# Optimization experiments

Hardware: AMD Instinct MI355X
Metric: run time of the kernel (lower is better)

## Reference

```python
import jax, jax.numpy as jnp
import numpy as np

B, T, C, H = 8, 1024, 1024, 16  # batch, seq, n_embd, n_head


def setup_inputs() -> dict:
    key = jax.random.key(0)
    ks = jax.random.split(key, 5)
    scale = 1.0 / np.sqrt(C)
    return {
        "x": jax.random.normal(ks[0], (B, T, C), dtype=jnp.float32),
        "Wqkv": jax.random.normal(ks[1], (C, 3 * C), dtype=jnp.float32) * scale,
        "bqkv": jax.random.normal(ks[2], (3 * C,), dtype=jnp.float32) * 0.02,
        "Wproj": jax.random.normal(ks[3], (C, C), dtype=jnp.float32) * scale,
        "bproj": jax.random.normal(ks[4], (C,), dtype=jnp.float32) * 0.02,
        "n_head": H,
    }


def reference(x, Wqkv, bqkv, Wproj, bproj, n_head):
    Bb, Tt, Cc = x.shape
    hd = Cc // n_head  # head dim
    qkv = x @ Wqkv + bqkv                      # [B,T,3C]
    q, k, v = jnp.split(qkv, 3, axis=-1)       # each [B,T,C]
    # [B,T,C] -> [B,H,T,hd]
    def to_heads(t):
        return t.reshape(Bb, Tt, n_head, hd).transpose(0, 2, 1, 3)
    q, k, v = to_heads(q), to_heads(k), to_heads(v)
    scores = jnp.einsum("bhqd,bhkd->bhqk", q, k) / jnp.sqrt(jnp.asarray(hd, q.dtype))
    causal = jnp.tril(jnp.ones((Tt, Tt), dtype=bool))
    scores = jnp.where(causal, scores, jnp.asarray(-jnp.inf, scores.dtype))
    attn = jax.nn.softmax(scores, axis=-1)
    y = jnp.einsum("bhqk,bhkd->bhqd", attn, v)  # [B,H,T,hd]
    y = y.transpose(0, 2, 1, 3).reshape(Bb, Tt, Cc)
    return y @ Wproj + bproj
```

## Files before the change

### kernel.cpp

```cpp
#include <hip/hip_runtime.h>
#include <hip/hip_bf16.h>
#include <math.h>
#include <type_traits>

#define Bz 8
#define Tz 1024
#define Cz 1024
#define Hz 16
#define HDz 64
#define Mz (Bz*Tz)
#define N1 (3*Cz)
#define QKN 2048

typedef __attribute__((ext_vector_type(8))) short short8;
typedef __attribute__((ext_vector_type(4))) short short4v;
typedef __attribute__((ext_vector_type(4))) float floatx4;

template<int V> using IC = std::integral_constant<int, V>;

__device__ __forceinline__ unsigned short f2bf(float f) {
    unsigned u = __float_as_uint(f);
    return (unsigned short)((u + 0x7FFFu + ((u >> 16) & 1u)) >> 16);
}

__device__ __forceinline__ unsigned pkbf(float a, float b) {
    __hip_bfloat162 h = __float22bfloat162_rn(make_float2(a, b));
    return *(unsigned*)&h;
}

__device__ __forceinline__ void gload16(const void* g, void* l) {
    __builtin_amdgcn_global_load_lds(
        (const __attribute__((address_space(1))) unsigned int*)g,
        (__attribute__((address_space(3))) unsigned int*)l, 16, 0, 0);
}

__global__ __launch_bounds__(256) void prep_kernel(
    const float* __restrict__ x, unsigned short* __restrict__ xb,
    const float* __restrict__ Wqkv, unsigned short* __restrict__ Wqkvt,
    const float* __restrict__ Wproj, unsigned short* __restrict__ Wprojt)
{
    __shared__ float tile[32][33];
    const int bid = blockIdx.x;
    const int tid = threadIdx.x;
    if (bid < 8192) {
        int i = bid * 256 + tid;
        float4 v = *(const float4*)&x[(size_t)i * 4];
        ushort4 o;
        o.x = f2bf(v.x); o.y = f2bf(v.y); o.z = f2bf(v.z); o.w = f2bf(v.w);
        *(ushort4*)&xb[(size_t)i * 4] = o;
        return;
    }
    const float* W; unsigned short* Wt; int K, N, n0, k0;
    if (bid < 11264) {
        int b = bid - 8192;  W = Wqkv;  Wt = Wqkvt;  K = Cz; N = N1;
        n0 = (b % 96) * 32;  k0 = (b / 96) * 32;
    } else {
        int b = bid - 11264; W = Wproj; Wt = Wprojt; K = Cz; N = Cz;
        n0 = (b % 32) * 32;  k0 = (b / 32) * 32;
    }
    const int tx = tid & 31, ty = tid >> 5;
#pragma unroll
    for (int i = 0; i < 4; ++i)
        tile[ty + i * 8][tx] = W[(size_t)(k0 + ty + i * 8) * N + n0 + tx];
    __syncthreads();
#pragma unroll
    for (int i = 0; i < 4; ++i)
        Wt[(size_t)(n0 + ty + i * 8) * K + k0 + tx] = f2bf(tile[tx][ty + i * 8]);
}

__global__ __launch_bounds__(512, 4) void gemm128_qkv(
    const unsigned short* __restrict__ A,
    const unsigned short* __restrict__ Bt,
    const float* __restrict__ bias,
    unsigned short* __restrict__ Cqk, unsigned short* __restrict__ VtG)
{
    __shared__ unsigned short lds[2 * 20480];
    constexpr int NT = 16;

    const int tid = threadIdx.x;
    const int lane = tid & 63;
    const int w = tid >> 6;
    const int wm = w >> 2, wn = w & 3;
    const int quad = lane >> 4, m16 = lane & 15;
    const int sw7 = m16 & 7;

    int wg = blockIdx.x;
    wg = (wg & 7) * 128 + (wg >> 3);
    const int bx = wg & 15, by = wg >> 4;
    const int row0 = by * 128, col0 = bx * 192;

    const int srow = tid >> 3;
    const int scol = ((tid & 7) ^ (srow & 7)) * 8;
    const unsigned short* a0 = A  + (size_t)(row0 + srow) * Cz + scol;
    const unsigned short* b0 = Bt + (size_t)(col0 + srow) * Cz + scol;

    auto stageA = [&](int kt, int db) {
        unsigned short* d = &lds[db * 20480 + w * 512];
        gload16(a0 + kt * 64, d);
        gload16(a0 + kt * 64 + 64 * Cz, d + 4096);
    };
    auto stageB = [&](int kt, int db) {
        unsigned short* d = &lds[db * 20480 + 8192 + w * 512];
        gload16(b0 + kt * 64, d);
        gload16(b0 + kt * 64 + 64 * Cz, d + 4096);
        gload16(b0 + kt * 64 + 128 * Cz, d + 8192);
    };

    float bv[3];
#pragma unroll
    for (int ni = 0; ni < 3; ++ni)
        bv[ni] = bias[col0 + wn * 48 + ni * 16 + m16];
    asm volatile("s_waitcnt vmcnt(0)" ::: "memory");

    floatx4 acc[4][3];
#pragma unroll
    for (int mi = 0; mi < 4; ++mi)
#pragma unroll
        for (int ni = 0; ni < 3; ++ni)
            acc[mi][ni] = (floatx4){0.f, 0.f, 0.f, 0.f};

    stageA(0, 0); stageB(0, 0);
    stageB(1, 1);
    asm volatile("s_waitcnt vmcnt(3)" ::: "memory");
    asm volatile("s_barrier" ::: "memory");

    int b = 0;
#pragma unroll 1
    for (int kt = 0; kt < NT; ++kt, b ^= 1) {
        const unsigned short* lA = &lds[b * 20480];
        const unsigned short* lB = &lds[b * 20480 + 8192];

        short8 bfr[3][2];
#pragma unroll
        for (int ni = 0; ni < 3; ++ni) {
            const int rb = wn * 48 + ni * 16 + m16;
#pragma unroll
            for (int ks = 0; ks < 2; ++ks)
                bfr[ni][ks] = *(const short8*)&lB[(rb >> 6) * 4096 + (rb & 63) * 64
                                                  + ((((ks << 2) | quad) ^ sw7) << 3)];
        }
        short8 af[2][2];
#pragma unroll
        for (int jj = 0; jj < 2; ++jj)
#pragma unroll
            for (int ks = 0; ks < 2; ++ks)
                af[jj][ks] = *(const short8*)&lA[wm * 4096 + (jj * 16 + m16) * 64
                                                 + ((((ks << 2) | quad) ^ sw7) << 3)];
        if (kt + 1 < NT) stageA(kt + 1, b ^ 1);
        asm volatile("s_barrier" ::: "memory");
        asm volatile("s_waitcnt lgkmcnt(0)" ::: "memory");
        __builtin_amdgcn_sched_barrier(0);
        __builtin_amdgcn_s_setprio(1);
#pragma unroll
        for (int ks = 0; ks < 2; ++ks)
#pragma unroll
            for (int jj = 0; jj < 2; ++jj)
#pragma unroll
                for (int ni = 0; ni < 3; ++ni)
                    acc[jj][ni] = __builtin_amdgcn_mfma_f32_16x16x32_bf16(
                        af[jj][ks], bfr[ni][ks], acc[jj][ni], 0, 0, 0);
        __builtin_amdgcn_s_setprio(0);
        asm volatile("s_barrier" ::: "memory");

        short8 af2[2][2];
#pragma unroll
        for (int jj = 0; jj < 2; ++jj)
#pragma unroll
            for (int ks = 0; ks < 2; ++ks)
                af2[jj][ks] = *(const short8*)&lA[wm * 4096 + ((2 + jj) * 16 + m16) * 64
                                                  + ((((ks << 2) | quad) ^ sw7) << 3)];
        if (kt + 2 < NT) stageB(kt + 2, b);
        asm volatile("s_barrier" ::: "memory");
        asm volatile("s_waitcnt lgkmcnt(0)" ::: "memory");
        __builtin_amdgcn_sched_barrier(0);
        __builtin_amdgcn_s_setprio(1);
#pragma unroll
        for (int ks = 0; ks < 2; ++ks)
#pragma unroll
            for (int jj = 0; jj < 2; ++jj)
#pragma unroll
                for (int ni = 0; ni < 3; ++ni)
                    acc[2 + jj][ni] = __builtin_amdgcn_mfma_f32_16x16x32_bf16(
                        af2[jj][ks], bfr[ni][ks], acc[2 + jj][ni], 0, 0, 0);
        __builtin_amdgcn_s_setprio(0);
        if (kt < NT - 2) { asm volatile("s_waitcnt vmcnt(3)" ::: "memory"); }
        else             { asm volatile("s_waitcnt vmcnt(0)" ::: "memory"); }
        asm volatile("s_barrier" ::: "memory");
    }

#pragma unroll
    for (int ni = 0; ni < 3; ++ni) {
        const int c0 = col0 + wn * 48 + ni * 16;
        if (c0 < 2048) {
#pragma unroll
            for (int mi = 0; mi < 4; ++mi)
#pragma unroll
                for (int reg = 0; reg < 4; ++reg) {
                    const int r = row0 + wm * 64 + mi * 16 + quad * 4 + reg;
                    Cqk[(size_t)r * QKN + c0 + m16] = f2bf(acc[mi][ni][reg] + bv[ni]);
                }
        } else {
            const int cb = c0 - 2048;
            const int hsel = cb >> 6;
            const int dd = (cb & 63) + m16;
            const int bq = row0 >> 10;
            const int tb = row0 & 1023;
            unsigned short* drow = VtG
                + (size_t)(bq * Hz + hsel) * (HDz * Tz)
                + (size_t)dd * Tz + tb;
#pragma unroll
            for (int mi = 0; mi < 4; ++mi) {
                const int t = wm * 64 + mi * 16 + quad * 4;
                unsigned pk[2];
                pk[0] = pkbf(acc[mi][ni][0] + bv[ni], acc[mi][ni][1] + bv[ni]);
                pk[1] = pkbf(acc[mi][ni][2] + bv[ni], acc[mi][ni][3] + bv[ni]);
                *(uint2*)&drow[t] = *(uint2*)pk;
            }
        }
    }
}

template<int NI, int MODE, int NXB>
__global__ __launch_bounds__(512) void gemm8p(
    const unsigned short* __restrict__ A,
    const unsigned short* __restrict__ Bt,
    const float* __restrict__ bias,
    void* __restrict__ Cout, unsigned short* __restrict__ VtG)
{
    constexpr int LDSB = 16384 + NI * 4096;
    constexpr int NT = 16;
    constexpr int NBLK = (Mz / 256) * NXB;
    constexpr int CHUNK = NBLK / 8;
    constexpr int NOUT = NXB * NI * 64;
    __shared__ unsigned short lds[2 * LDSB];

    const int tid = threadIdx.x;
    const int lane = tid & 63;
    const int w = tid >> 6;
    const int wm = w >> 2, wn = w & 3;
    const int quad = lane >> 4, m16 = lane & 15;
    const int sw7 = m16 & 7;

    int wg = blockIdx.x;
    wg = (wg & 7) * CHUNK + (wg >> 3);
    const int bx = wg % NXB, by = wg / NXB;
    const int row0 = by * 256, col0 = bx * (NI * 64);

    const int srow = tid >> 3;
    const int scol = ((tid & 7) ^ (srow & 7)) * 8;
    const unsigned short* sA[2][2];
    const unsigned short* sBu[NI];
#pragma unroll
    for (int h = 0; h < 2; ++h)
#pragma unroll
        for (int c = 0; c < 2; ++c)
            sA[h][c] = A + (size_t)(row0 + h * 128 + c * 64 + srow) * Cz + scol;
#pragma unroll
    for (int u = 0; u < NI; ++u)
        sBu[u] = Bt + (size_t)(col0 + u * 64 + srow) * Cz + scol;

    auto stage_tile = [&](int kt, int db) {
        unsigned short* base = &lds[db * LDSB];
#pragma unroll
        for (int u = 0; u < NI; ++u)
            gload16(sBu[u] + kt * 64, base + 16384 + u * 4096 + w * 512);
        gload16(sA[0][0] + kt * 64, base + w * 512);
        gload16(sA[0][1] + kt * 64, base + w * 512 + 4096);
        gload16(sA[1][0] + kt * 64, base + 8192 + w * 512);
        gload16(sA[1][1] + kt * 64, base + 8192 + w * 512 + 4096);
    };

    float bv[NI];
#pragma unroll
    for (int ni = 0; ni < NI; ++ni)
        bv[ni] = bias[col0 + wn * (NI * 16) + ni * 16 + m16];
    asm volatile("s_waitcnt vmcnt(0)" ::: "memory");

    floatx4 acc[8][NI];
#pragma unroll
    for (int mi = 0; mi < 8; ++mi)
#pragma unroll
        for (int ni = 0; ni < NI; ++ni)
            acc[mi][ni] = (floatx4){0.f, 0.f, 0.f, 0.f};

    stage_tile(0, 0);
    stage_tile(1, 1);

    int b = 0;
#pragma unroll 1
    for (int kt = 0; kt < NT; ++kt, b ^= 1) {
        if (kt < NT - 1) {
            if constexpr (NI == 3) asm volatile("s_waitcnt vmcnt(7)" ::: "memory");
            else                   asm volatile("s_waitcnt vmcnt(6)" ::: "memory");
        } else {
            asm volatile("s_waitcnt vmcnt(0)" ::: "memory");
        }
        asm volatile("s_barrier" ::: "memory");

        const unsigned short* lA = &lds[b * LDSB];
        const unsigned short* lB = &lds[b * LDSB + 16384];

        auto loadA = [&](auto pc, short8 (&af)[2][2]) {
            constexpr int p = decltype(pc)::value;
            constexpr int hf = p >> 1;
#pragma unroll
            for (int j = 0; j < 2; ++j) {
                const int ra = ((p & 1) * 64 + j * 32 + wm * 16 + m16) * 64;
#pragma unroll
                for (int ks = 0; ks < 2; ++ks)
                    af[j][ks] = *(const short8*)&lA[hf * 8192 + ra + ((((ks << 2) | quad) ^ sw7) << 3)];
            }
        };

        short8 bfr[NI][2];
#pragma unroll
        for (int ni = 0; ni < NI; ++ni) {
            const int rb = (wn * (NI * 16) + ni * 16 + m16) * 64;
#pragma unroll
            for (int ks = 0; ks < 2; ++ks)
                bfr[ni][ks] = *(const short8*)&lB[rb + ((((ks << 2) | quad) ^ sw7) << 3)];
        }

        auto cluster = [&](auto pc, short8 (&af)[2][2]) {
            constexpr int p = decltype(pc)::value;
            __builtin_amdgcn_s_setprio(1);
#pragma unroll
            for (int ks = 0; ks < 2; ++ks)
#pragma unroll
                for (int j = 0; j < 2; ++j)
#pragma unroll
                    for (int ni = 0; ni < NI; ++ni)
                        acc[p * 2 + j][ni] = __builtin_amdgcn_mfma_f32_16x16x32_bf16(
                            af[j][ks], bfr[ni][ks], acc[p * 2 + j][ni], 0, 0, 0);
            __builtin_amdgcn_s_setprio(0);
        };

        short8 afA[2][2], afB[2][2];
        loadA(IC<0>{}, afA);
        __builtin_amdgcn_sched_barrier(0);
        loadA(IC<1>{}, afB);
        __builtin_amdgcn_sched_barrier(0);
        asm volatile("s_waitcnt lgkmcnt(4)" ::: "memory");
        __builtin_amdgcn_sched_barrier(0);
        cluster(IC<0>{}, afA);
        loadA(IC<2>{}, afA);
        __builtin_amdgcn_sched_barrier(0);
        asm volatile("s_waitcnt lgkmcnt(4)" ::: "memory");
        __builtin_amdgcn_sched_barrier(0);
        cluster(IC<1>{}, afB);
        loadA(IC<3>{}, afB);
        __builtin_amdgcn_sched_barrier(0);
        asm volatile("s_waitcnt lgkmcnt(4)" ::: "memory");
        __builtin_amdgcn_sched_barrier(0);
        cluster(IC<2>{}, afA);
        asm volatile("s_waitcnt lgkmcnt(0)" ::: "memory");
        __builtin_amdgcn_sched_barrier(0);
        if (kt + 2 < NT) {
            asm volatile("s_barrier" ::: "memory");
            stage_tile(kt + 2, b);
        }
        __builtin_amdgcn_sched_barrier(0);
        cluster(IC<3>{}, afB);
    }

    if constexpr (MODE == 0) {
#pragma unroll
        for (int ni = 0; ni < NI; ++ni) {
            const int c = col0 + wn * (NI * 16) + ni * 16 + m16;
#pragma unroll
            for (int mi = 0; mi < 8; ++mi)
#pragma unroll
                for (int reg = 0; reg < 4; ++reg) {
                    const int r = row0 + mi * 32 + wm * 16 + quad * 4 + reg;
                    ((float*)Cout)[(size_t)r * NOUT + c] = acc[mi][ni][reg] + bv[ni];
                }
        }
    } else {
#pragma unroll
        for (int ni = 0; ni < NI; ++ni) {
            const int c0 = col0 + wn * (NI * 16) + ni * 16;
            if (c0 < 2048) {
#pragma unroll
                for (int mi = 0; mi < 8; ++mi)
#pragma unroll
                    for (int reg = 0; reg < 4; ++reg) {
                        const int r = row0 + mi * 32 + wm * 16 + quad * 4 + reg;
                        ((unsigned short*)Cout)[(size_t)r * QKN + c0 + m16] =
                            f2bf(acc[mi][ni][reg] + bv[ni]);
                    }
            } else {
                const int cb = c0 - 2048;
                const int hsel = cb >> 6;
                const int dd = (cb & 63) + m16;
                const int bq = row0 >> 10;
                const int tb = row0 & 1023;
                unsigned short* drow = VtG
                    + (size_t)(bq * Hz + hsel) * (HDz * Tz)
                    + (size_t)dd * Tz + tb;
#pragma unroll
                for (int mi = 0; mi < 8; ++mi) {
                    const int t = mi * 32 + wm * 16 + quad * 4;
                    unsigned pk[2];
                    pk[0] = pkbf(acc[mi][ni][0] + bv[ni], acc[mi][ni][1] + bv[ni]);
                    pk[1] = pkbf(acc[mi][ni][2] + bv[ni], acc[mi][ni][3] + bv[ni]);
                    *(uint2*)&drow[t] = *(uint2*)pk;
                }
            }
        }
    }
}

__global__ __launch_bounds__(128) void attn_kernel(const unsigned short* __restrict__ qkb,
    const unsigned short* __restrict__ VtG, unsigned short* __restrict__ attb)
{
    __shared__ unsigned short Ks[2][64 * 64];
    __shared__ unsigned short Vs[2][64 * 64];

    const int bid = blockIdx.x;
    const int qi = 15 - (bid >> 7);
    const int bh = bid & 127;
    const int b = bh >> 4, h = bh & 15;
    const int tid = threadIdx.x, lane = tid & 63, w = tid >> 6;
    const int quad = lane >> 4, m16 = lane & 15;

    const unsigned short* Kb = qkb + (size_t)(b * Tz) * QKN + Cz + h * HDz;
    const unsigned short* Vb = VtG + (size_t)bh * (HDz * Tz);

    const int l3 = lane >> 3, l7 = lane & 7;
    const int gsw = ((l7 ^ l3) << 3);
    const int sw = m16 & 7;
    const int p0 = (quad ^ sw) << 3;

    short8 onesf = (short8){0,0,0,0,0,0,0,0};
    if (m16 == 0) {
        const short one = (short)0x3F80;
        onesf = (short8){one,one,one,one,one,one,one,one};
    }

    int srow[4];
#pragma unroll
    for (int i = 0; i < 4; ++i) srow[i] = w * 32 + i * 8 + l3;

#pragma unroll
    for (int i = 0; i < 4; ++i) {
        gload16(Kb + (size_t)srow[i] * QKN + gsw, &Ks[0][(w * 4 + i) * 512]);
        gload16(Vb + (size_t)srow[i] * Tz + gsw, &Vs[0][(w * 4 + i) * 512]);
    }

    short8 qf[2][2];
    int qrow[2];
#pragma unroll
    for (int mi = 0; mi < 2; ++mi) {
        qrow[mi] = qi * 64 + w * 32 + mi * 16 + m16;
        const size_t rq = (size_t)(b * Tz + qrow[mi]) * QKN + h * HDz;
        qf[mi][0] = *(const short8*)&qkb[rq + quad * 8];
        qf[mi][1] = *(const short8*)&qkb[rq + 32 + quad * 8];
    }

    floatx4 of[2][4];
#pragma unroll
    for (int mi = 0; mi < 2; ++mi)
#pragma unroll
        for (int dc = 0; dc < 4; ++dc) of[mi][dc] = (floatx4){0.f, 0.f, 0.f, 0.f};
    floatx4 lsum[2];
    lsum[0] = (floatx4){0.f, 0.f, 0.f, 0.f};
    lsum[1] = (floatx4){0.f, 0.f, 0.f, 0.f};

    int buf = 0;

    auto tile_body = [&](auto diag_c) {
        constexpr bool DIAG = decltype(diag_c)::value;
        short8 pf[2][2];
#pragma unroll
        for (int m0 = 0; m0 < 4; ++m0) {
            if (DIAG && w == 0 && m0 >= 2) continue;
            const unsigned short* kr = &Ks[buf][(m0 * 16 + m16) * 64];
            short8 kf0 = *(const short8*)&kr[p0];
            short8 kf1 = *(const short8*)&kr[p0 ^ 32];
#pragma unroll
            for (int mi = 0; mi < 2; ++mi) {
                floatx4 st = (floatx4){0.f, 0.f, 0.f, 0.f};
                st = __builtin_amdgcn_mfma_f32_16x16x32_bf16(kf0, qf[mi][0], st, 0, 0, 0);
                st = __builtin_amdgcn_mfma_f32_16x16x32_bf16(kf1, qf[mi][1], st, 0, 0, 0);
                float p[4];
#pragma unroll
                for (int reg = 0; reg < 4; ++reg) {
                    p[reg] = exp2f(st[reg] * 0.18033688f);
                    if (DIAG) {
                        int key = m0 * 16 + quad * 4 + reg;
                        int qr  = w * 32 + mi * 16 + m16;
                        p[reg] = (key <= qr) ? p[reg] : 0.f;
                    }
                }
                unsigned* pp = (unsigned*)&pf[mi][m0 >> 1];
                pp[(m0 & 1) * 2 + 0] = pkbf(p[0], p[1]);
                pp[(m0 & 1) * 2 + 1] = pkbf(p[2], p[3]);
            }
        }
#pragma unroll
        for (int kg = 0; kg < 2; ++kg) {
            if (DIAG && w == 0 && kg == 1) continue;
#pragma unroll
            for (int mi = 0; mi < 2; ++mi)
                lsum[mi] = __builtin_amdgcn_mfma_f32_16x16x32_bf16(onesf, pf[mi][kg], lsum[mi], 0, 0, 0);
#pragma unroll
            for (int dc = 0; dc < 4; ++dc) {
                const unsigned short* vrow = &Vs[buf][(dc * 16 + m16) * 64];
                const int g0 = kg * 4 + (quad >> 1);
                const int off = (quad & 1) * 4;
                short4v v0 = *(const short4v*)&vrow[((g0 ^ sw) << 3) + off];
                short4v v1 = *(const short4v*)&vrow[(((g0 + 2) ^ sw) << 3) + off];
                short8 vf;
                vf[0] = v0[0]; vf[1] = v0[1]; vf[2] = v0[2]; vf[3] = v0[3];
                vf[4] = v1[0]; vf[5] = v1[1]; vf[6] = v1[2]; vf[7] = v1[3];
#pragma unroll
                for (int mi = 0; mi < 2; ++mi)
                    of[mi][dc] = __builtin_amdgcn_mfma_f32_16x16x32_bf16(vf, pf[mi][kg], of[mi][dc], 0, 0, 0);
            }
        }
    };

    for (int ki = 0; ki <= qi; ++ki) {
        __syncthreads();
        if (ki < qi) {
            const size_t ko = (size_t)(ki + 1) * 64;
#pragma unroll
            for (int i = 0; i < 4; ++i) {
                gload16(Kb + (ko + srow[i]) * QKN + gsw, &Ks[buf ^ 1][(w * 4 + i) * 512]);
                gload16(Vb + (size_t)srow[i] * Tz + ko + gsw, &Vs[buf ^ 1][(w * 4 + i) * 512]);
            }
        }
        if (ki == qi) tile_body(std::true_type{});
        else          tile_body(std::false_type{});
        buf ^= 1;
    }

#pragma unroll
    for (int mi = 0; mi < 2; ++mi) {
        const float l = __shfl(lsum[mi][0], m16);
        const float inv = 1.f / l;
        const size_t orow = (size_t)(b * Tz + qrow[mi]) * Cz + h * HDz;
#pragma unroll
        for (int dc = 0; dc < 4; ++dc) {
            ushort4 o;
            o.x = f2bf(of[mi][dc][0] * inv);
            o.y = f2bf(of[mi][dc][1] * inv);
            o.z = f2bf(of[mi][dc][2] * inv);
            o.w = f2bf(of[mi][dc][3] * inv);
            *(ushort4*)&attb[orow + dc * 16 + quad * 4] = o;
        }
    }
}

extern "C" void kernel_launch(void* const* d_in, const int* in_sizes, int n_in,
                              void* d_out, int out_size, void* d_ws, size_t ws_size,
                              hipStream_t stream)
{
    const float* x     = (const float*)d_in[0];
    const float* Wqkv  = (const float*)d_in[1];
    const float* bqkv  = (const float*)d_in[2];
    const float* Wproj = (const float*)d_in[3];
    const float* bproj = (const float*)d_in[4];
    float* out = (float*)d_out;

    unsigned short* xb     = (unsigned short*)d_ws;
    unsigned short* Wqkvt  = xb + (size_t)Mz * Cz;
    unsigned short* Wprojt = Wqkvt + (size_t)N1 * Cz;
    unsigned short* qkb    = Wprojt + (size_t)Cz * Cz;
    unsigned short* VtG    = qkb + (size_t)Mz * QKN;
    unsigned short* attb   = xb;

    prep_kernel<<<12288, 256, 0, stream>>>(x, xb, Wqkv, Wqkvt, Wproj, Wprojt);

    gemm128_qkv<<<1024, 512, 0, stream>>>(xb, Wqkvt, bqkv, qkb, VtG);

    attn_kernel<<<2048, 128, 0, stream>>>(qkb, VtG, attb);

    gemm8p<2, 0, 8><<<256, 512, 0, stream>>>(attb, Wprojt, bproj, out, nullptr);
}
```

Measured before the change: 225.1 us.

## Load K and V fragments directly from global memory instead of LDS staging

The attention kernel drops its double-buffered LDS staging of K and V tiles and the per-tile __syncthreads, and has each lane read its MFMA operand fragments straight from global memory (relying on L1/L2). It also adds a launch-bounds occupancy hint of 4 blocks and splits the loop so only the final tile takes the diagonal-mask path. This removes barrier and LDS traffic overhead, but the two waves now each fetch K/V separately. The loads are also less coalesced and no longer overlap with compute through prefetch, which can expose global latency.

After: 274.7 us. +22.0%, slower.

```diff
diff --git a/kernel.cpp b/kernel.cpp
--- a/kernel.cpp
+++ b/kernel.cpp
@@ -410,12 +410,9 @@
     }
 }
 
-__global__ __launch_bounds__(128) void attn_kernel(const unsigned short* __restrict__ qkb,
+__global__ __launch_bounds__(128, 4) void attn_kernel(const unsigned short* __restrict__ qkb,
     const unsigned short* __restrict__ VtG, unsigned short* __restrict__ attb)
 {
-    __shared__ unsigned short Ks[2][64 * 64];
-    __shared__ unsigned short Vs[2][64 * 64];
-
     const int bid = blockIdx.x;
     const int qi = 15 - (bid >> 7);
     const int bh = bid & 127;
@@ -426,25 +423,10 @@
     const unsigned short* Kb = qkb + (size_t)(b * Tz) * QKN + Cz + h * HDz;
     const unsigned short* Vb = VtG + (size_t)bh * (HDz * Tz);
 
-    const int l3 = lane >> 3, l7 = lane & 7;
-    const int gsw = ((l7 ^ l3) << 3);
-    const int sw = m16 & 7;
-    const int p0 = (quad ^ sw) << 3;
-
     short8 onesf = (short8){0,0,0,0,0,0,0,0};
     if (m16 == 0) {
         const short one = (short)0x3F80;
         onesf = (short8){one,one,one,one,one,one,one,one};
-    }
-
-    int srow[4];
-#pragma unroll
-    for (int i = 0; i < 4; ++i) srow[i] = w * 32 + i * 8 + l3;
-
-#pragma unroll
-    for (int i = 0; i < 4; ++i) {
-        gload16(Kb + (size_t)srow[i] * QKN + gsw, &Ks[0][(w * 4 + i) * 512]);
-        gload16(Vb + (size_t)srow[i] * Tz + gsw, &Vs[0][(w * 4 + i) * 512]);
     }
 
     short8 qf[2][2];
@@ -466,17 +448,18 @@
     lsum[0] = (floatx4){0.f, 0.f, 0.f, 0.f};
     lsum[1] = (floatx4){0.f, 0.f, 0.f, 0.f};
 
-    int buf = 0;
-
-    auto tile_body = [&](auto diag_c) {
+    const unsigned short* krow = Kb + (size_t)m16 * QKN + quad * 8;
+    const unsigned short* vrow = Vb + (size_t)m16 * Tz + quad * 4;
+
+    auto tile_body = [&](const int kt, auto diag_c) {
         constexpr bool DIAG = decltype(diag_c)::value;
         short8 pf[2][2];
 #pragma unroll
         for (int m0 = 0; m0 < 4; ++m0) {
             if (DIAG && w == 0 && m0 >= 2) continue;
-            const unsigned short* kr = &Ks[buf][(m0 * 16 + m16) * 64];
-            short8 kf0 = *(const short8*)&kr[p0];
-            short8 kf1 = *(const short8*)&kr[p0 ^ 32];
+            const unsigned short* kr = krow + (size_t)(kt * 64 + m0 * 16) * QKN;
+            short8 kf0 = *(const short8*)kr;
+            short8 kf1 = *(const short8*)(kr + 32);
 #pragma unroll
             for (int mi = 0; mi < 2; ++mi) {
                 floatx4 st = (floatx4){0.f, 0.f, 0.f, 0.f};
@@ -505,11 +488,9 @@
                 lsum[mi] = __builtin_amdgcn_mfma_f32_16x16x32_bf16(onesf, pf[mi][kg], lsum[mi], 0, 0, 0);
 #pragma unroll
             for (int dc = 0; dc < 4; ++dc) {
-                const unsigned short* vrow = &Vs[buf][(dc * 16 + m16) * 64];
-                const int g0 = kg * 4 + (quad >> 1);
-                const int off = (quad & 1) * 4;
-                short4v v0 = *(const short4v*)&vrow[((g0 ^ sw) << 3) + off];
-                short4v v1 = *(const short4v*)&vrow[(((g0 + 2) ^ sw) << 3) + off];
+                const unsigned short* vr = vrow + (size_t)(dc * 16) * Tz + kt * 64 + kg * 32;
+                short4v v0 = *(const short4v*)vr;
+                short4v v1 = *(const short4v*)(vr + 16);
                 short8 vf;
                 vf[0] = v0[0]; vf[1] = v0[1]; vf[2] = v0[2]; vf[3] = v0[3];
                 vf[4] = v1[0]; vf[5] = v1[1]; vf[6] = v1[2]; vf[7] = v1[3];
@@ -520,20 +501,9 @@
         }
     };
 
-    for (int ki = 0; ki <= qi; ++ki) {
-        __syncthreads();
-        if (ki < qi) {
-            const size_t ko = (size_t)(ki + 1) * 64;
-#pragma unroll
-            for (int i = 0; i < 4; ++i) {
-                gload16(Kb + (ko + srow[i]) * QKN + gsw, &Ks[buf ^ 1][(w * 4 + i) * 512]);
-                gload16(Vb + (size_t)srow[i] * Tz + ko + gsw, &Vs[buf ^ 1][(w * 4 + i) * 512]);
-            }
-        }
-        if (ki == qi) tile_body(std::true_type{});
-        else          tile_body(std::false_type{});
-        buf ^= 1;
-    }
+#pragma unroll 1
+    for (int ki = 0; ki < qi; ++ki) tile_body(ki, std::false_type{});
+    tile_body(qi, std::true_type{});
 
 #pragma unroll
     for (int mi = 0; mi < 2; ++mi) {
```
